# Performance work log

Hardware: AMD Instinct MI355X
Metric: run time of the kernel (lower is better)

The kernel has to match this reference:

```python
import jax, jax.numpy as jnp
import numpy as np
import math

B, T = 16, 512
P = 256          # num_memory_positions
E = 128          # embedding_dim
NB = 4           # num_beings
K = 4            # attention_radius
TEMP = 8.0       # attention_temperature
PHI = 1.618033988749895


def setup_inputs() -> dict:
    key = jax.random.key(0)
    ks = jax.random.split(key, 8)
    x = jax.random.normal(ks[0], (B, T, 8), jnp.float32)
    W_in = jax.random.normal(ks[1], (8, E), jnp.float32) * 0.1
    b_in = jnp.zeros((E,), jnp.float32)
    W_out = jax.random.normal(ks[2], (E, 8), jnp.float32) * 0.1
    b_out = jnp.zeros((8,), jnp.float32)
    W_p = jax.random.normal(ks[3], (E, E), jnp.float32) * (1.0 / np.sqrt(E))
    b_p = jnp.zeros((E,), jnp.float32)
    ptr_dest = jax.random.uniform(ks[4], (NB, P), jnp.float32) * P
    jump_W = jax.random.normal(ks[5], (NB, E), jnp.float32) * 0.1
    jump_b = jnp.zeros((NB,), jnp.float32)
    ctx_strength = jnp.full((NB,), 0.2, jnp.float32)
    pe = np.zeros((NB, E), np.float32)
    for i in range(NB):
        ph = i * PHI
        v = []
        for h in range(1, 9):
            v += [math.sin(h * ph), math.cos(h * ph)]
        pe[i, :16] = v  # phase_embedding padded with zeros to E (E >= 16)
    phase_bias = jnp.asarray(pe)
    seg = P / NB
    pointer_init = jax.random.uniform(ks[6], (NB, B), jnp.float32) * seg + jnp.arange(NB, dtype=jnp.float32)[:, None] * seg
    return dict(x=x, W_in=W_in, b_in=b_in, W_out=W_out, b_out=b_out,
                W_p=W_p, b_p=b_p, ptr_dest=ptr_dest, jump_W=jump_W,
                jump_b=jump_b, ctx_strength=ctx_strength,
                phase_bias=phase_bias, pointer_init=pointer_init)


def _forward(x, W_in, b_in, W_out, b_out, W_p, b_p, ptr_dest, jump_W,
             jump_b, ctx_strength, phase_bias, pointer_init):
    offsets = jnp.arange(-K, K + 1)          # [W]
    b_ix = jnp.arange(B)                     # [B]
    half = P / 2.0
    ring0 = jnp.zeros((B, P, E), x.dtype)
    hid0 = jnp.zeros((NB, B, E), x.dtype)

    def step(carry, x_t):
        ring, ptrs, hids = carry
        inp = x_t @ W_in + b_in              # [B,E]
        outs, new_ptrs, new_hids = [], [], []
        for i in range(NB):                  # beings sequential (share ring)
            ptr, hid = ptrs[i], hids[i]
            base = jnp.clip(jnp.floor(ptr).astype(jnp.int32), 0, P - 1)
            idx = (base[:, None] + offsets[None, :]) % P            # [B,W]
            delta = jnp.mod(idx.astype(x_t.dtype) - ptr[:, None] + half, P) - half
            w = jax.nn.softmax(-(delta ** 2) / TEMP, axis=1)         # [B,W]
            nbhd = ring[b_ix[:, None], idx]                          # [B,W,E]
            ctx = jnp.sum(w[..., None] * nbhd, axis=1)               # [B,E]
            comb = inp + jax.nn.sigmoid(ctx_strength[i]) * ctx + 0.1 * phase_bias[i]
            s = jnp.tanh(comb + hid)
            s = jnp.tanh(s @ W_p + b_p)      # depth-1 = 1 processing layer
            ring = ring.at[b_ix[:, None], idx].add(w[..., None] * s[:, None, :])
            cur = jnp.clip(ptr.astype(jnp.int32), 0, P - 1)
            jump_target = ptr_dest[i][cur]                           # [B]
            probs = jax.nn.sigmoid(s @ jump_W[i] + jump_b[i])        # [B]
            hard = (probs > 0.5).astype(s.dtype)
            should_jump = hard - jax.lax.stop_gradient(probs) + probs
            walk = (ptr + 1.0) % P
            new_ptrs.append(jnp.where(should_jump > 0.5, jump_target, walk))
            new_hids.append(s)
            outs.append(s @ W_out + b_out)                           # [B,8]
        out_t = jnp.mean(jnp.stack(outs), axis=0)                    # [B,8] (training-mode mean)
        return (ring, jnp.stack(new_ptrs), jnp.stack(new_hids)), out_t

    _, ys = jax.lax.scan(step, (ring0, pointer_init, hid0), jnp.swapaxes(x, 0, 1))
    return jnp.swapaxes(ys, 0, 1)            # [B,T,8]


def reference(x, W_in, b_in, W_out, b_out, W_p, b_p, ptr_dest, jump_W,
              jump_b, ctx_strength, phase_bias, pointer_init):
    return _forward(x, W_in, b_in, W_out, b_out, W_p, b_p, ptr_dest,
                    jump_W, jump_b, ctx_strength, phase_bias, pointer_init)
```

## Files before the change

kernel.cpp:

```cpp
#include <hip/hip_runtime.h>
#include <cmath>

namespace {
constexpr int B_ = 16, T_ = 512, P_ = 256, E_ = 128, NB_ = 4, K_ = 4;

__device__ __forceinline__ float rcpf(float x) { return __builtin_amdgcn_rcpf(x); }
__device__ __forceinline__ float fast_tanh(float x) {
    float a = fabsf(x);
    float t = __expf(-2.0f * a);
    float r = 1.0f - 2.0f * t * rcpf(1.0f + t);
    return copysignf(r, x);
}
}

__global__ __launch_bounds__(256, 1)
void swarm_ring_kernel(const float* __restrict__ x,
                       const float* __restrict__ W_in,
                       const float* __restrict__ b_in,
                       const float* __restrict__ W_out,
                       const float* __restrict__ b_out,
                       const float* __restrict__ W_p,
                       const float* __restrict__ b_p,
                       const float* __restrict__ ptr_dest,
                       const float* __restrict__ jump_W,
                       const float* __restrict__ jump_b,
                       const float* __restrict__ ctx_strength,
                       const float* __restrict__ phase_bias,
                       const float* __restrict__ pointer_init,
                       float* __restrict__ out)
{
    __shared__ alignas(16) float  ring[P_ * E_];
    __shared__ alignas(16) float  s_buf[2 * E_];
    __shared__ alignas(16) float4 s4[E_];
    __shared__ alignas(16) float  red[16];
    __shared__ alignas(16) float  hist[16][132];
    __shared__ alignas(16) float  wout_s[8][132];

    const int tid   = threadIdx.x;
    const int b     = blockIdx.x;
    const int wave  = tid >> 6;
    const int lane  = tid & 63;
    const int khalf = lane >> 5;
    const int e     = (wave << 5) | (lane & 31);

    for (int k4 = tid; k4 < P_ * E_ / 4; k4 += 256)
        ((float4*)ring)[k4] = make_float4(0.f, 0.f, 0.f, 0.f);
    for (int idx = tid; idx < 8 * E_; idx += 256) {
        const int m = idx >> 7, ee = idx & 127;
        wout_s[m][ee] = W_out[ee * 8 + m] * 0.25f;
    }

    float wp[64];
    #pragma unroll
    for (int kk = 0; kk < 64; ++kk)
        wp[kk] = W_p[(khalf * 64 + kk) * E_ + e];

    const float bin_r = b_in[e];
    const float bp_r  = b_p[e];
    float win_r[8];
    #pragma unroll
    for (int k = 0; k < 8; ++k) win_r[k] = W_in[k * E_ + e];
    const float bout_m = b_out[tid & 7];

    float pb_r[NB_], jw_r[NB_], sigc[NB_], jb_r[NB_], hid[NB_], ptrv[NB_];
    #pragma unroll
    for (int i = 0; i < NB_; ++i) {
        pb_r[i] = 0.1f * phase_bias[i * E_ + e];
        jw_r[i] = jump_W[i * E_ + e];
        sigc[i] = 1.0f / (1.0f + __expf(-ctx_strength[i]));
        jb_r[i] = jump_b[i];
        hid[i]  = 0.0f;
        ptrv[i] = pointer_init[i * B_ + b];
    }

    const float* xb = x + (size_t)b * T_ * 8;
    float xt[8];
    {
        float4 a0 = ((const float4*)xb)[0], a1 = ((const float4*)xb)[1];
        xt[0]=a0.x; xt[1]=a0.y; xt[2]=a0.z; xt[3]=a0.w;
        xt[4]=a1.x; xt[5]=a1.y; xt[6]=a1.z; xt[7]=a1.w;
    }

    const float Cw1 = 0.8824969f, Cw2 = 0.60653066f, Cw3 = 0.32465247f, Cw4 = 0.13533528f;
    const float Dw1 = 0.7788008f, Dw2 = 0.36787944f, Dw3 = 0.105399225f, Dw4 = 0.018315639f;

    __syncthreads();

    for (int t = 0; t < T_; ++t) {
        int   baseA[NB_];
        float fA[NB_], psinv[NB_], jt[NB_], wgt[NB_][9];
        #pragma unroll
        for (int i = 0; i < NB_; ++i) {
            const float p = ptrv[i];
            const int base = (int)p;
            baseA[i] = base;
            jt[i] = ptr_dest[i * P_ + base];
            const float f = p - (float)base;
            fA[i] = f;
            const float r  = __expf(0.25f * f);
            const float r2 = r * r, r3 = r2 * r, r4 = r2 * r2;
            const float ri = rcpf(r), ri2 = ri * ri, ri3 = ri2 * ri, ri4 = ri2 * ri2;
            const float p0 = Cw4*ri4, p1 = Cw3*ri3, p2 = Cw2*ri2, p3 = Cw1*ri, p4 = 1.0f,
                        p5 = Cw1*r,  p6 = Cw2*r2,  p7 = Cw3*r3,  p8 = Cw4*r4;
            const float sum = ((p0+p1)+(p2+p3)) + ((p4+p5)+(p6+p7)) + p8;
            const float inv = rcpf(sum);
            psinv[i] = inv;
            wgt[i][0]=p0*inv; wgt[i][1]=p1*inv; wgt[i][2]=p2*inv; wgt[i][3]=p3*inv;
            wgt[i][4]=p4*inv; wgt[i][5]=p5*inv; wgt[i][6]=p6*inv; wgt[i][7]=p7*inv;
            wgt[i][8]=p8*inv;
        }

        int ddm[NB_][NB_];
        bool overlap = false;
        #pragma unroll
        for (int j = 1; j < NB_; ++j)
            #pragma unroll
            for (int i = 0; i < j; ++i) {
                const int dd = ((baseA[j] - baseA[i] + 128) & 255) - 128;
                ddm[j][i] = dd;
                overlap = overlap || (dd >= -8 && dd <= 8);
            }

        float ctxp[NB_];
        #pragma unroll
        for (int i = 0; i < NB_; ++i) {
            float c = 0.f;
            #pragma unroll
            for (int u = 0; u < 5; ++u) {
                const float wlo = wgt[i][u];
                const float whi = (u == 0) ? 0.f : wgt[i][u + 4];
                const float wv  = khalf ? whi : wlo;
                const int row = (baseA[i] + u + (khalf << 2) - K_) & (P_ - 1);
                c = fmaf(wv, ring[row * E_ + e], c);
            }
            c += __shfl_xor(c, 32);
            ctxp[i] = c;
        }

        float inp = bin_r;
        #pragma unroll
        for (int k = 0; k < 8; ++k) inp = fmaf(xt[k], win_r[k], inp);

        float xtn[8];
        if (t + 1 < T_) {
            float4 a0 = ((const float4*)(xb + (t + 1) * 8))[0];
            float4 a1 = ((const float4*)(xb + (t + 1) * 8))[1];
            xtn[0]=a0.x; xtn[1]=a0.y; xtn[2]=a0.z; xtn[3]=a0.w;
            xtn[4]=a1.x; xtn[5]=a1.y; xtn[6]=a1.z; xtn[7]=a1.w;
        } else {
            #pragma unroll
            for (int k = 0; k < 8; ++k) xtn[k] = 0.f;
        }

        float sv[NB_];

        if (!overlap) {
            float s1v[NB_];
            #pragma unroll
            for (int j = 0; j < NB_; ++j)
                s1v[j] = fast_tanh(fmaf(sigc[j], ctxp[j], inp + pb_r[j] + hid[j]));
            if (lane < 32)
                s4[e] = make_float4(s1v[0], s1v[1], s1v[2], s1v[3]);
            __syncthreads();

            float a0 = 0.f, a1 = 0.f, a2 = 0.f, a3 = 0.f;
            const float4* sp = s4 + khalf * 64;
            #pragma unroll
            for (int kk = 0; kk < 64; ++kk) {
                const float4 sb = sp[kk];
                const float w = wp[kk];
                a0 = fmaf(sb.x, w, a0);
                a1 = fmaf(sb.y, w, a1);
                a2 = fmaf(sb.z, w, a2);
                a3 = fmaf(sb.w, w, a3);
            }
            a0 += __shfl_xor(a0, 32);
            a1 += __shfl_xor(a1, 32);
            a2 += __shfl_xor(a2, 32);
            a3 += __shfl_xor(a3, 32);
            sv[0] = fast_tanh(a0 + bp_r);
            sv[1] = fast_tanh(a1 + bp_r);
            sv[2] = fast_tanh(a2 + bp_r);
            sv[3] = fast_tanh(a3 + bp_r);
            #pragma unroll
            for (int j = 0; j < NB_; ++j) hid[j] = sv[j];

            #pragma unroll
            for (int j = 0; j < NB_; ++j) {
                const int o0 = (baseA[j] ^ khalf) & 1;
                #pragma unroll
                for (int u = 0; u < 4; ++u) {
                    const float wv = o0 ? wgt[j][2 * u + 1] : wgt[j][2 * u];
                    const int r = (baseA[j] + 2 * u + o0 - K_) & (P_ - 1);
                    ring[r * E_ + e] += wv * sv[j];
                }
                if (o0 == 0) {
                    const int r = (baseA[j] + 8 - K_) & (P_ - 1);
                    ring[r * E_ + e] += wgt[j][8] * sv[j];
                }
            }
        } else {
            float coefm[NB_][NB_];
            #pragma unroll
            for (int j = 1; j < NB_; ++j) {
                #pragma unroll
                for (int i = 0; i < j; ++i) {
                    const int dd = ddm[j][i];
                    float c = 0.f;
                    if (dd >= -8 && dd <= 8) {
                        const float A = (float)dd - fA[i];
                        const float s  = __expf(-0.25f * (A - fA[j]));
                        const float G  = __expf(0.125f * (fA[i] * fA[i] - A * A));
                        const float s2p = s * s, s3p = s2p * s, s4p = s2p * s2p;
                        const float si = rcpf(s), si2 = si * si, si3 = si2 * si, si4 = si2 * si2;
                        float acc = 0.f;
                        acc += (dd >= 0)              ? Dw4 * si4 : 0.f;
                        acc += (dd >= -1 && dd <= 7)  ? Dw3 * si3 : 0.f;
                        acc += (dd >= -2 && dd <= 6)  ? Dw2 * si2 : 0.f;
                        acc += (dd >= -3 && dd <= 5)  ? Dw1 * si  : 0.f;
                        acc += (dd >= -4 && dd <= 4)  ? 1.0f      : 0.f;
                        acc += (dd >= -5 && dd <= 3)  ? Dw1 * s   : 0.f;
                        acc += (dd >= -6 && dd <= 2)  ? Dw2 * s2p : 0.f;
                        acc += (dd >= -7 && dd <= 1)  ? Dw3 * s3p : 0.f;
                        acc += (dd <= 0)              ? Dw4 * s4p : 0.f;
                        c = psinv[i] * psinv[j] * G * acc;
                    }
                    coefm[j][i] = c;
                }
            }

            #pragma unroll
            for (int j = 0; j < NB_; ++j) {
                float ctx = ctxp[j];
                #pragma unroll
                for (int i = 0; i < j; ++i) ctx = fmaf(coefm[j][i], sv[i], ctx);
                const float s1 = fast_tanh(fmaf(sigc[j], ctx, inp + pb_r[j] + hid[j]));
                if (lane < 32) s_buf[(j & 1) * E_ + e] = s1;
                __syncthreads();

                const float4* sp = (const float4*)(s_buf + (j & 1) * E_ + khalf * 64);
                float acc = 0.f;
                #pragma unroll
                for (int k4 = 0; k4 < 16; ++k4) {
                    const float4 sq = sp[k4];
                    acc = fmaf(sq.x, wp[4 * k4 + 0], acc);
                    acc = fmaf(sq.y, wp[4 * k4 + 1], acc);
                    acc = fmaf(sq.z, wp[4 * k4 + 2], acc);
                    acc = fmaf(sq.w, wp[4 * k4 + 3], acc);
                }
                acc += __shfl_xor(acc, 32);
                const float s2 = fast_tanh(acc + bp_r);
                sv[j] = s2; hid[j] = s2;

                const int o0 = (baseA[j] ^ khalf) & 1;
                #pragma unroll
                for (int u = 0; u < 4; ++u) {
                    const float wv = o0 ? wgt[j][2 * u + 1] : wgt[j][2 * u];
                    const int r = (baseA[j] + 2 * u + o0 - K_) & (P_ - 1);
                    ring[r * E_ + e] += wv * s2;
                }
                if (o0 == 0) {
                    const int r = (baseA[j] + 8 - K_) & (P_ - 1);
                    ring[r * E_ + e] += wgt[j][8] * s2;
                }
            }
        }

        {
            float va = khalf ? sv[2] * jw_r[2] : sv[0] * jw_r[0];
            float vb = khalf ? sv[3] * jw_r[3] : sv[1] * jw_r[1];
            #pragma unroll
            for (int off = 1; off < 32; off <<= 1) {
                va += __shfl_xor(va, off);
                vb += __shfl_xor(vb, off);
            }
            if ((lane & 31) == 0)
                ((float2*)red)[wave * 2 + khalf] = make_float2(va, vb);
        }

        {
            const float ssum = (sv[0] + sv[1]) + (sv[2] + sv[3]);
            if (lane < 32) hist[t & 15][e] = ssum;
        }

        __syncthreads();

        {
            const float4 r0 = ((const float4*)red)[0];
            const float4 r1 = ((const float4*)red)[1];
            const float4 r2 = ((const float4*)red)[2];
            const float4 r3 = ((const float4*)red)[3];
            const float zz[4] = {
                ((r0.x + r1.x) + (r2.x + r3.x)) + jb_r[0],
                ((r0.y + r1.y) + (r2.y + r3.y)) + jb_r[1],
                ((r0.z + r1.z) + (r2.z + r3.z)) + jb_r[2],
                ((r0.w + r1.w) + (r2.w + r3.w)) + jb_r[3]};
            #pragma unroll
            for (int i = 0; i < NB_; ++i) {
                float np;
                if (zz[i] > 0.0f) np = jt[i];
                else { np = ptrv[i] + 1.0f; if (np >= 256.0f) np -= 256.0f; }
                ptrv[i] = np;
            }
        }

        if ((t & 7) == 7 && tid < 64) {
            const int tt = tid >> 3;
            const int m  = tid & 7;
            const float* hrow = hist[(t - 7 + tt) & 15];
            const float* wrow = wout_s[m];
            float acc = 0.f;
            #pragma unroll
            for (int q = 0; q < 32; ++q) {
                const float4 h4 = ((const float4*)hrow)[q];
                const float4 w4 = ((const float4*)wrow)[q];
                acc += ((h4.x * w4.x + h4.y * w4.y) + (h4.z * w4.z + h4.w * w4.w));
            }
            out[((size_t)b * T_ + (t - 7 + tt)) * 8 + m] = acc + bout_m;
        }

        #pragma unroll
        for (int k = 0; k < 8; ++k) xt[k] = xtn[k];
    }
}

extern "C" void kernel_launch(void* const* d_in, const int* in_sizes, int n_in,
                              void* d_out, int out_size, void* d_ws, size_t ws_size,
                              hipStream_t stream) {
    (void)in_sizes; (void)n_in; (void)out_size; (void)d_ws; (void)ws_size;
    swarm_ring_kernel<<<dim3(B_), dim3(256), 0, stream>>>(
        (const float*)d_in[0],  (const float*)d_in[1],  (const float*)d_in[2],
        (const float*)d_in[3],  (const float*)d_in[4],  (const float*)d_in[5],
        (const float*)d_in[6],  (const float*)d_in[7],  (const float*)d_in[8],
        (const float*)d_in[9],  (const float*)d_in[10], (const float*)d_in[11],
        (const float*)d_in[12], (float*)d_out);
}
```

Measured before the change: 2.147 ms.

## Remap threads to two embedding columns each with a four-way K split

Each thread now owns two adjacent embedding columns (float2) instead of one, and the K reduction of the W_p matvec is split four ways across 16-lane groups instead of two ways. The ring gather, ring scatter and matvec use float2 shared-memory accesses, with a two-step shuffle reduction replacing the single cross-half shuffle. The aim is fewer LDS instructions per FMA and less per-thread serial matvec work on the latency-bound recurrence, at the cost of more shuffles and redundant elementwise tanh work across the four lanes of each group. W_in is now reread from global memory every step instead of kept in registers.

Result: faster. 2.058 ms (-4.1%).

```diff
diff --git a/kernel.cpp b/kernel.cpp
--- a/kernel.cpp
+++ b/kernel.cpp
@@ -10,6 +10,16 @@
     float t = __expf(-2.0f * a);
     float r = 1.0f - 2.0f * t * rcpf(1.0f + t);
     return copysignf(r, x);
+}
+__device__ __forceinline__ float redkq(float v) {
+    v += __shfl_xor(v, 16);
+    v += __shfl_xor(v, 32);
+    return v;
+}
+__device__ __forceinline__ float sel4(int kq, float a, float b, float c, float d) {
+    const float t0 = (kq & 1) ? b : a;
+    const float t1 = (kq & 1) ? d : c;
+    return (kq & 2) ? t1 : t0;
 }
 }
 
@@ -30,18 +40,19 @@
                        float* __restrict__ out)
 {
     __shared__ alignas(16) float  ring[P_ * E_];
-    __shared__ alignas(16) float  s_buf[2 * E_];
     __shared__ alignas(16) float4 s4[E_];
+    __shared__ alignas(16) float  sbuf[2 * E_];
     __shared__ alignas(16) float  red[16];
     __shared__ alignas(16) float  hist[16][132];
     __shared__ alignas(16) float  wout_s[8][132];
 
-    const int tid   = threadIdx.x;
-    const int b     = blockIdx.x;
-    const int wave  = tid >> 6;
-    const int lane  = tid & 63;
-    const int khalf = lane >> 5;
-    const int e     = (wave << 5) | (lane & 31);
+    const int tid = threadIdx.x;
+    const int b   = blockIdx.x;
+    const int w   = tid >> 6;
+    const int l   = tid & 63;
+    const int sub = l & 15;
+    const int kq  = l >> 4;
+    const int e0  = ((w << 4) | sub) << 1;
 
     for (int k4 = tid; k4 < P_ * E_ / 4; k4 += 256)
         ((float4*)ring)[k4] = make_float4(0.f, 0.f, 0.f, 0.f);
@@ -50,26 +61,25 @@
         wout_s[m][ee] = W_out[ee * 8 + m] * 0.25f;
     }
 
-    float wp[64];
+    float2 wp2[32];
     #pragma unroll
-    for (int kk = 0; kk < 64; ++kk)
-        wp[kk] = W_p[(khalf * 64 + kk) * E_ + e];
-
-    const float bin_r = b_in[e];
-    const float bp_r  = b_p[e];
-    float win_r[8];
-    #pragma unroll
-    for (int k = 0; k < 8; ++k) win_r[k] = W_in[k * E_ + e];
-    const float bout_m = b_out[tid & 7];
-
-    float pb_r[NB_], jw_r[NB_], sigc[NB_], jb_r[NB_], hid[NB_], ptrv[NB_];
+    for (int kk = 0; kk < 32; ++kk)
+        wp2[kk] = *(const float2*)(W_p + (kq * 32 + kk) * E_ + e0);
+
+    const float2 bin2 = *(const float2*)(b_in + e0);
+    const float2 bp2  = *(const float2*)(b_p + e0);
+    const float  bout_m = b_out[tid & 7];
+
+    float2 pb2[NB_], jw2[NB_], hid2[NB_];
+    float  sigc[NB_], jb_r[NB_], ptrv[NB_];
     #pragma unroll
     for (int i = 0; i < NB_; ++i) {
-        pb_r[i] = 0.1f * phase_bias[i * E_ + e];
-        jw_r[i] = jump_W[i * E_ + e];
+        const float2 pb = *(const float2*)(phase_bias + i * E_ + e0);
+        pb2[i] = make_float2(0.1f * pb.x, 0.1f * pb.y);
+        jw2[i] = *(const float2*)(jump_W + i * E_ + e0);
         sigc[i] = 1.0f / (1.0f + __expf(-ctx_strength[i]));
         jb_r[i] = jump_b[i];
-        hid[i]  = 0.0f;
+        hid2[i] = make_float2(0.f, 0.f);
         ptrv[i] = pointer_init[i * B_ + b];
     }
 
@@ -121,25 +131,34 @@
                 overlap = overlap || (dd >= -8 && dd <= 8);
             }
 
-        float ctxp[NB_];
+        float  ws0[NB_], ws1[NB_];
+        float2 ctxp2[NB_];
         #pragma unroll
         for (int i = 0; i < NB_; ++i) {
-            float c = 0.f;
-            #pragma unroll
-            for (int u = 0; u < 5; ++u) {
-                const float wlo = wgt[i][u];
-                const float whi = (u == 0) ? 0.f : wgt[i][u + 4];
-                const float wv  = khalf ? whi : wlo;
-                const int row = (baseA[i] + u + (khalf << 2) - K_) & (P_ - 1);
-                c = fmaf(wv, ring[row * E_ + e], c);
-            }
-            c += __shfl_xor(c, 32);
-            ctxp[i] = c;
-        }
-
-        float inp = bin_r;
-        #pragma unroll
-        for (int k = 0; k < 8; ++k) inp = fmaf(xt[k], win_r[k], inp);
+            ws0[i] = sel4(kq, wgt[i][0], wgt[i][1], wgt[i][2], wgt[i][3]);
+            ws1[i] = sel4(kq, wgt[i][4], wgt[i][5], wgt[i][6], wgt[i][7]);
+            const int r0 = (baseA[i] + kq - K_) & (P_ - 1);
+            const int r1 = (baseA[i] + kq + 4 - K_) & (P_ - 1);
+            const float2 g0 = *(const float2*)(ring + r0 * E_ + e0);
+            const float2 g1 = *(const float2*)(ring + r1 * E_ + e0);
+            float cx = fmaf(ws1[i], g1.x, ws0[i] * g0.x);
+            float cy = fmaf(ws1[i], g1.y, ws0[i] * g0.y);
+            if (kq == 0) {
+                const int r2 = (baseA[i] + 8 - K_) & (P_ - 1);
+                const float2 g2 = *(const float2*)(ring + r2 * E_ + e0);
+                cx = fmaf(wgt[i][8], g2.x, cx);
+                cy = fmaf(wgt[i][8], g2.y, cy);
+            }
+            ctxp2[i] = make_float2(redkq(cx), redkq(cy));
+        }
+
+        float2 inp2 = bin2;
+        #pragma unroll
+        for (int k = 0; k < 8; ++k) {
+            const float2 wk = *(const float2*)(W_in + k * E_ + e0);
+            inp2.x = fmaf(xt[k], wk.x, inp2.x);
+            inp2.y = fmaf(xt[k], wk.y, inp2.y);
+        }
 
         float xtn[8];
         if (t + 1 < T_) {
@@ -152,51 +171,58 @@
             for (int k = 0; k < 8; ++k) xtn[k] = 0.f;
         }
 
-        float sv[NB_];
+        float2 sv2[NB_];
 
         if (!overlap) {
-            float s1v[NB_];
-            #pragma unroll
-            for (int j = 0; j < NB_; ++j)
-                s1v[j] = fast_tanh(fmaf(sigc[j], ctxp[j], inp + pb_r[j] + hid[j]));
-            if (lane < 32)
-                s4[e] = make_float4(s1v[0], s1v[1], s1v[2], s1v[3]);
+            float2 s1v[NB_];
+            #pragma unroll
+            for (int j = 0; j < NB_; ++j) {
+                s1v[j].x = fast_tanh(fmaf(sigc[j], ctxp2[j].x, inp2.x + pb2[j].x + hid2[j].x));
+                s1v[j].y = fast_tanh(fmaf(sigc[j], ctxp2[j].y, inp2.y + pb2[j].y + hid2[j].y));
+            }
+            if (kq == 0) {
+                s4[e0]     = make_float4(s1v[0].x, s1v[1].x, s1v[2].x, s1v[3].x);
+                s4[e0 + 1] = make_float4(s1v[0].y, s1v[1].y, s1v[2].y, s1v[3].y);
+            }
             __syncthreads();
 
-            float a0 = 0.f, a1 = 0.f, a2 = 0.f, a3 = 0.f;
-            const float4* sp = s4 + khalf * 64;
-            #pragma unroll
-            for (int kk = 0; kk < 64; ++kk) {
-                const float4 sb = sp[kk];
-                const float w = wp[kk];
-                a0 = fmaf(sb.x, w, a0);
-                a1 = fmaf(sb.y, w, a1);
-                a2 = fmaf(sb.z, w, a2);
-                a3 = fmaf(sb.w, w, a3);
-            }
-            a0 += __shfl_xor(a0, 32);
-            a1 += __shfl_xor(a1, 32);
-            a2 += __shfl_xor(a2, 32);
-            a3 += __shfl_xor(a3, 32);
-            sv[0] = fast_tanh(a0 + bp_r);
-            sv[1] = fast_tanh(a1 + bp_r);
-            sv[2] = fast_tanh(a2 + bp_r);
-            sv[3] = fast_tanh(a3 + bp_r);
-            #pragma unroll
-            for (int j = 0; j < NB_; ++j) hid[j] = sv[j];
+            float2 ab0 = make_float2(0.f, 0.f), ab1 = ab0, ab2 = ab0, ab3 = ab0;
+            const float4* sp = s4 + kq * 32;
+            #pragma unroll
+            for (int kk = 0; kk < 32; ++kk) {
+                const float4 sq = sp[kk];
+                const float2 w2 = wp2[kk];
+                ab0.x = fmaf(sq.x, w2.x, ab0.x); ab0.y = fmaf(sq.x, w2.y, ab0.y);
+                ab1.x = fmaf(sq.y, w2.x, ab1.x); ab1.y = fmaf(sq.y, w2.y, ab1.y);
+                ab2.x = fmaf(sq.z, w2.x, ab2.x); ab2.y = fmaf(sq.z, w2.y, ab2.y);
+                ab3.x = fmaf(sq.w, w2.x, ab3.x); ab3.y = fmaf(sq.w, w2.y, ab3.y);
+            }
+            sv2[0] = make_float2(fast_tanh(redkq(ab0.x) + bp2.x), fast_tanh(redkq(ab0.y) + bp2.y));
+            sv2[1] = make_float2(fast_tanh(redkq(ab1.x) + bp2.x), fast_tanh(redkq(ab1.y) + bp2.y));
+            sv2[2] = make_float2(fast_tanh(redkq(ab2.x) + bp2.x), fast_tanh(redkq(ab2.y) + bp2.y));
+            sv2[3] = make_float2(fast_tanh(redkq(ab3.x) + bp2.x), fast_tanh(redkq(ab3.y) + bp2.y));
+            #pragma unroll
+            for (int j = 0; j < NB_; ++j) hid2[j] = sv2[j];
 
             #pragma unroll
             for (int j = 0; j < NB_; ++j) {
-                const int o0 = (baseA[j] ^ khalf) & 1;
-                #pragma unroll
-                for (int u = 0; u < 4; ++u) {
-                    const float wv = o0 ? wgt[j][2 * u + 1] : wgt[j][2 * u];
-                    const int r = (baseA[j] + 2 * u + o0 - K_) & (P_ - 1);
-                    ring[r * E_ + e] += wv * sv[j];
-                }
-                if (o0 == 0) {
-                    const int r = (baseA[j] + 8 - K_) & (P_ - 1);
-                    ring[r * E_ + e] += wgt[j][8] * sv[j];
+                const float2 s = sv2[j];
+                const int r0 = (baseA[j] + kq - K_) & (P_ - 1);
+                float2* q0 = (float2*)(ring + r0 * E_ + e0);
+                float2 v0 = *q0;
+                v0.x = fmaf(ws0[j], s.x, v0.x); v0.y = fmaf(ws0[j], s.y, v0.y);
+                *q0 = v0;
+                const int r1 = (baseA[j] + kq + 4 - K_) & (P_ - 1);
+                float2* q1 = (float2*)(ring + r1 * E_ + e0);
+                float2 v1 = *q1;
+                v1.x = fmaf(ws1[j], s.x, v1.x); v1.y = fmaf(ws1[j], s.y, v1.y);
+                *q1 = v1;
+                if (kq == 0) {
+                    const int r2 = (baseA[j] + 8 - K_) & (P_ - 1);
+                    float2* q2 = (float2*)(ring + r2 * E_ + e0);
+                    float2 v2 = *q2;
+                    v2.x = fmaf(wgt[j][8], s.x, v2.x); v2.y = fmaf(wgt[j][8], s.y, v2.y);
+                    *q2 = v2;
                 }
             }
         } else {
@@ -231,56 +257,76 @@
 
             #pragma unroll
             for (int j = 0; j < NB_; ++j) {
-                float ctx = ctxp[j];
+                float2 ctx = ctxp2[j];
                 #pragma unroll
-                for (int i = 0; i < j; ++i) ctx = fmaf(coefm[j][i], sv[i], ctx);
-                const float s1 = fast_tanh(fmaf(sigc[j], ctx, inp + pb_r[j] + hid[j]));
-                if (lane < 32) s_buf[(j & 1) * E_ + e] = s1;
+                for (int i = 0; i < j; ++i) {
+                    ctx.x = fmaf(coefm[j][i], sv2[i].x, ctx.x);
+                    ctx.y = fmaf(coefm[j][i], sv2[i].y, ctx.y);
+                }
+                float2 s1;
+                s1.x = fast_tanh(fmaf(sigc[j], ctx.x, inp2.x + pb2[j].x + hid2[j].x));
+                s1.y = fast_tanh(fmaf(sigc[j], ctx.y, inp2.y + pb2[j].y + hid2[j].y));
+                if (kq == 0) *(float2*)(sbuf + (j & 1) * E_ + e0) = s1;
                 __syncthreads();
 
-                const float4* sp = (const float4*)(s_buf + (j & 1) * E_ + khalf * 64);
-                float acc = 0.f;
+                const float4* sp = (const float4*)(sbuf + (j & 1) * E_) + kq * 8;
+                float ax = 0.f, ay = 0.f;
                 #pragma unroll
-                for (int k4 = 0; k4 < 16; ++k4) {
-                    const float4 sq = sp[k4];
-                    acc = fmaf(sq.x, wp[4 * k4 + 0], acc);
-                    acc = fmaf(sq.y, wp[4 * k4 + 1], acc);
-                    acc = fmaf(sq.z, wp[4 * k4 + 2], acc);
-                    acc = fmaf(sq.w, wp[4 * k4 + 3], acc);
-                }
-                acc += __shfl_xor(acc, 32);
-                const float s2 = fast_tanh(acc + bp_r);
-                sv[j] = s2; hid[j] = s2;
-
-                const int o0 = (baseA[j] ^ khalf) & 1;
-                #pragma unroll
-                for (int u = 0; u < 4; ++u) {
-                    const float wv = o0 ? wgt[j][2 * u + 1] : wgt[j][2 * u];
-                    const int r = (baseA[j] + 2 * u + o0 - K_) & (P_ - 1);
-                    ring[r * E_ + e] += wv * s2;
-                }
-                if (o0 == 0) {
-                    const int r = (baseA[j] + 8 - K_) & (P_ - 1);
-                    ring[r * E_ + e] += wgt[j][8] * s2;
+                for (int kk = 0; kk < 8; ++kk) {
+                    const float4 sq = sp[kk];
+                    const float2 wa = wp2[4 * kk + 0], wb = wp2[4 * kk + 1];
+                    const float2 wc = wp2[4 * kk + 2], wd = wp2[4 * kk + 3];
+                    ax = fmaf(sq.x, wa.x, ax); ay = fmaf(sq.x, wa.y, ay);
+                    ax = fmaf(sq.y, wb.x, ax); ay = fmaf(sq.y, wb.y, ay);
+                    ax = fmaf(sq.z, wc.x, ax); ay = fmaf(sq.z, wc.y, ay);
+                    ax = fmaf(sq.w, wd.x, ax); ay = fmaf(sq.w, wd.y, ay);
+                }
+                float2 s2;
+                s2.x = fast_tanh(redkq(ax) + bp2.x);
+                s2.y = fast_tanh(redkq(ay) + bp2.y);
+                sv2[j] = s2; hid2[j] = s2;
+
+                const int r0 = (baseA[j] + kq - K_) & (P_ - 1);
+                float2* q0 = (float2*)(ring + r0 * E_ + e0);
+                float2 v0 = *q0;
+                v0.x = fmaf(ws0[j], s2.x, v0.x); v0.y = fmaf(ws0[j], s2.y, v0.y);
+                *q0 = v0;
+                const int r1 = (baseA[j] + kq + 4 - K_) & (P_ - 1);
+                float2* q1 = (float2*)(ring + r1 * E_ + e0);
+                float2 v1 = *q1;
+                v1.x = fmaf(ws1[j], s2.x, v1.x); v1.y = fmaf(ws1[j], s2.y, v1.y);
+                *q1 = v1;
+                if (kq == 0) {
+                    const int r2 = (baseA[j] + 8 - K_) & (P_ - 1);
+                    float2* q2 = (float2*)(ring + r2 * E_ + e0);
+                    float2 v2 = *q2;
+                    v2.x = fmaf(wgt[j][8], s2.x, v2.x); v2.y = fmaf(wgt[j][8], s2.y, v2.y);
+                    *q2 = v2;
                 }
             }
         }
 
         {
-            float va = khalf ? sv[2] * jw_r[2] : sv[0] * jw_r[0];
-            float vb = khalf ? sv[3] * jw_r[3] : sv[1] * jw_r[1];
-            #pragma unroll
-            for (int off = 1; off < 32; off <<= 1) {
-                va += __shfl_xor(va, off);
-                vb += __shfl_xor(vb, off);
-            }
-            if ((lane & 31) == 0)
-                ((float2*)red)[wave * 2 + khalf] = make_float2(va, vb);
+            float vj0 = fmaf(sv2[0].y, jw2[0].y, sv2[0].x * jw2[0].x);
+            float vj1 = fmaf(sv2[1].y, jw2[1].y, sv2[1].x * jw2[1].x);
+            float vj2 = fmaf(sv2[2].y, jw2[2].y, sv2[2].x * jw2[2].x);
+            float vj3 = fmaf(sv2[3].y, jw2[3].y, sv2[3].x * jw2[3].x);
+            #pragma unroll
+            for (int off = 1; off < 16; off <<= 1) {
+                vj0 += __shfl_xor(vj0, off);
+                vj1 += __shfl_xor(vj1, off);
+                vj2 += __shfl_xor(vj2, off);
+                vj3 += __shfl_xor(vj3, off);
+            }
+            if (l == 0)
+                ((float4*)red)[w] = make_float4(vj0, vj1, vj2, vj3);
         }
 
         {
-            const float ssum = (sv[0] + sv[1]) + (sv[2] + sv[3]);
-            if (lane < 32) hist[t & 15][e] = ssum;
+            float2 ssum2;
+            ssum2.x = (sv2[0].x + sv2[1].x) + (sv2[2].x + sv2[3].x);
+            ssum2.y = (sv2[0].y + sv2[1].y) + (sv2[2].y + sv2[3].y);
+            if (kq == 0) *(float2*)(&hist[t & 15][e0]) = ssum2;
         }
 
         __syncthreads();
```
